# Kernel tuning notes

Hardware: AMD Instinct MI355X
Metric: run time of the kernel (lower is better)

Reference implementation:

```python
import jax, jax.numpy as jnp
import numpy as np

N = 128            # grid points per dim (periodic)
BS = 32            # batch size
MAX_ITERS = 8      # outer hybrid-solver iterations
HINTS_PERIOD = 4   # ML expert used every 4th iteration (HINTS schedule)
HIDDEN = 64        # CNN hidden channels
H = 1.0 / N        # grid spacing


def _laplacian(u):
    # periodic 5-point Laplacian on [..., N, N]
    return (
        jnp.roll(u, 1, axis=-1) + jnp.roll(u, -1, axis=-1)
        + jnp.roll(u, 1, axis=-2) + jnp.roll(u, -1, axis=-2)
        - 4.0 * u
    ) / (H * H)


def _pconv(x, w, b):
    # periodic-padded 3x3 conv, NCHW / OIHW
    xp = jnp.pad(x, ((0, 0), (0, 0), (1, 1), (1, 1)), mode='wrap')
    y = jax.lax.conv_general_dilated(xp, w, (1, 1), 'VALID',
                                     dimension_numbers=('NCHW', 'OIHW', 'NCHW'))
    return y + b[None, :, None, None]


def _cnn(x, w1, b1, w2, b2, w3, b3):
    # ML expert: residual [bs,1,N,N] -> correction [bs,1,N,N]
    h = jax.nn.relu(_pconv(x, w1, b1))
    h = jax.nn.relu(_pconv(h, w2, b2))
    return _pconv(h, w3, b3)


def setup_inputs() -> dict:
    key = jax.random.key(0)
    ks = jax.random.split(key, 7)
    f = jax.random.normal(ks[0], (BS, N, N), dtype=jnp.float32)
    u0 = jnp.zeros((BS, N, N), dtype=jnp.float32)
    s1 = 1.0 / np.sqrt(1 * 9)
    s2 = 1.0 / np.sqrt(HIDDEN * 9)
    w1 = jax.random.normal(ks[1], (HIDDEN, 1, 3, 3), jnp.float32) * s1
    b1 = jnp.zeros((HIDDEN,), jnp.float32)
    w2 = jax.random.normal(ks[2], (HIDDEN, HIDDEN, 3, 3), jnp.float32) * s2
    b2 = jnp.zeros((HIDDEN,), jnp.float32)
    w3 = jax.random.normal(ks[3], (1, HIDDEN, 3, 3), jnp.float32) * s2
    b3 = jnp.zeros((1,), jnp.float32)
    return {'f': f, 'u0': u0, 'w1': w1, 'b1': b1, 'w2': w2, 'b2': b2,
            'w3': w3, 'b3': b3}


def reference(f, u0, w1, b1, w2, b2, w3, b3):
    one_hot_ml = jnp.array([0.0, 1.0], dtype=jnp.float32)
    one_hot_num = jnp.array([1.0, 0.0], dtype=jnp.float32)

    def step(u, it):
        # residual of -lap(u) = f  ->  r = f + lap(u)
        res = f + _laplacian(u)
        # expert 0: one Jacobi sweep (diag of -lap is 4/h^2)
        u_num = u + (H * H / 4.0) * res
        # expert 1: ML correction on residual
        u_ml = u + _cnn(res[:, None], w1, b1, w2, b2, w3, b3)[:, 0]
        # HINTS router: ML every HINTS_PERIOD-th iteration, same for all samples
        use_ml = (it % HINTS_PERIOD) == (HINTS_PERIOD - 1)
        u_new = jnp.where(use_ml, u_ml, u_num)
        scores = jnp.broadcast_to(
            jnp.where(use_ml, one_hot_ml, one_hot_num)[None, :], (BS, 2))
        return u_new, (u_new, scores)

    _, (predictions, routing_scores) = jax.lax.scan(
        step, u0, jnp.arange(MAX_ITERS))
    # predictions: [max_iters, bs, N, N]; routing_scores: [max_iters, bs, 2]
    return predictions, routing_scores
```

## Files before the change

### kernel.cpp

```cpp
#include <hip/hip_runtime.h>
#include <hip/hip_bf16.h>

#define BS 32
#define SPAT 16384
#define NMASK 127

using short8  = __attribute__((ext_vector_type(8))) short;
using short4v = __attribute__((ext_vector_type(4))) short;
using f32x16  = __attribute__((ext_vector_type(16))) float;
using f32x4   = __attribute__((ext_vector_type(4))) float;

__device__ inline short f2bf(float f) {
  __hip_bfloat16 h = __float2bfloat16(f);
  return *reinterpret_cast<short*>(&h);
}

__global__ __launch_bounds__(256) void prep_kernel(
    const float* __restrict__ w2, const float* __restrict__ w1,
    const float* __restrict__ w3, short* __restrict__ w2b,
    short* __restrict__ w1a, short* __restrict__ w3b) {
  int idx = blockIdx.x * 256 + threadIdx.x;
  if (idx < 36864) {
    int cob = idx / 18432, r = idx % 18432;
    int t = r / 2048, r2 = r & 2047;
    int c = r2 >> 9, lh = (r2 >> 8) & 1, l31 = (r2 >> 3) & 31, j = r2 & 7;
    int co = cob * 32 + l31, ci = c * 16 + 8 * lh + j;
    w2b[idx] = f2bf(w2[(co * 64 + ci) * 9 + t]);
  } else if (idx < 37888) {
    int j = idx - 36864;
    int ch = j >> 4, t = j & 15;
    w1a[j] = (t < 9) ? f2bf(w1[ch * 9 + t]) : (short)0;
  } else if (idx < 39936) {
    int q = idx - 37888;
    int c = q >> 9, lh = (q >> 8) & 1, l31 = (q >> 3) & 31, j = q & 7;
    int t = l31, ci = c * 16 + 8 * lh + j;
    w3b[q] = (t < 9) ? f2bf(w3[ci * 9 + t]) : (short)0;
  }
}

__global__ __launch_bounds__(256) void jac3_kernel(
    const float* __restrict__ uin, const float* __restrict__ f,
    float* __restrict__ u1o, float* __restrict__ u2o,
    float* __restrict__ u3o, float* __restrict__ res_ws) {
  __shared__ float As[576];
  __shared__ float Bs[484];
  __shared__ float Fs[484];
  int tid = threadIdx.x;
  int bl = blockIdx.x >> 6, tile = blockIdx.x & 63;
  int y0 = (tile >> 3) << 4, x0 = (tile & 7) << 4;
  const float* ub = uin + ((size_t)bl << 14);
  const float* fb = f + ((size_t)bl << 14);
  for (int i = tid; i < 576; i += 256) {
    int uy = i / 24, ux = i % 24;
    As[i] = ub[(((y0 + uy - 4) & NMASK) << 7) + ((x0 + ux - 4) & NMASK)];
  }
  for (int i = tid; i < 484; i += 256) {
    int uy = i / 22, ux = i % 22;
    Fs[i] = fb[(((y0 + uy - 3) & NMASK) << 7) + ((x0 + ux - 3) & NMASK)];
  }
  __syncthreads();
  for (int i = tid; i < 484; i += 256) {
    int yy = i / 22, xx = i % 22;
    float uc = As[(yy + 1) * 24 + xx + 1];
    float ns = As[yy * 24 + xx + 1] + As[(yy + 2) * 24 + xx + 1]
             + As[(yy + 1) * 24 + xx] + As[(yy + 1) * 24 + xx + 2];
    Bs[i] = uc + Fs[i] * (1.f / 65536.f) + (ns - 4.f * uc) * 0.25f;
  }
  __syncthreads();
  {
    int y = tid >> 4, x = tid & 15;
    u1o[((size_t)bl << 14) + ((y0 + y) << 7) + x0 + x] = Bs[(y + 3) * 22 + x + 3];
  }
  for (int i = tid; i < 400; i += 256) {
    int yy = i / 20, xx = i % 20;
    float uc = Bs[(yy + 1) * 22 + xx + 1];
    float ns = Bs[yy * 22 + xx + 1] + Bs[(yy + 2) * 22 + xx + 1]
             + Bs[(yy + 1) * 22 + xx] + Bs[(yy + 1) * 22 + xx + 2];
    As[i] = uc + Fs[(yy + 1) * 22 + xx + 1] * (1.f / 65536.f)
          + (ns - 4.f * uc) * 0.25f;
  }
  __syncthreads();
  {
    int y = tid >> 4, x = tid & 15;
    u2o[((size_t)bl << 14) + ((y0 + y) << 7) + x0 + x] = As[(y + 2) * 20 + x + 2];
  }
  for (int i = tid; i < 324; i += 256) {
    int yy = i / 18, xx = i % 18;
    float uc = As[(yy + 1) * 20 + xx + 1];
    float ns = As[yy * 20 + xx + 1] + As[(yy + 2) * 20 + xx + 1]
             + As[(yy + 1) * 20 + xx] + As[(yy + 1) * 20 + xx + 2];
    Bs[i] = uc + Fs[(yy + 2) * 22 + xx + 2] * (1.f / 65536.f)
          + (ns - 4.f * uc) * 0.25f;
  }
  __syncthreads();
  {
    int y = tid >> 4, x = tid & 15;
    size_t gi = ((size_t)bl << 14) + ((y0 + y) << 7) + x0 + x;
    float uc = Bs[(y + 1) * 18 + x + 1];
    u3o[gi] = uc;
    float ns = Bs[y * 18 + x + 1] + Bs[(y + 2) * 18 + x + 1]
             + Bs[(y + 1) * 18 + x] + Bs[(y + 1) * 18 + x + 2];
    res_ws[gi] = Fs[(y + 3) * 22 + x + 3] + (ns - 4.f * uc) * 16384.f;
  }
}

__global__ __launch_bounds__(512, 6) void mlstep_a(
    const float* __restrict__ res_ws,
    const short* __restrict__ w1a, const float* __restrict__ b1v,
    const short* __restrict__ w2b, const float* __restrict__ b2v,
    const short* __restrict__ w3b, float* __restrict__ D_ws,
    int b0, int BC) {
  __shared__ __align__(16) short h1g[8 * 324 * 8];
  __shared__ float res_s[400];
  int tid = threadIdx.x;
  int bl = blockIdx.x >> 6;
  int tile = blockIdx.x & 63;
  int y0 = (tile >> 3) << 4, x0 = (tile & 7) << 4;
  const float* rb = res_ws + ((size_t)(b0 + bl) << 14);

  if (tid < 400) {
    int ry = tid / 20, rx = tid % 20;
    res_s[tid] = rb[(((y0 + ry - 2) & NMASK) << 7) + ((x0 + rx - 2) & NMASK)];
  }
  __syncthreads();

  int lane = tid & 63, wv = tid >> 6;
  int l31 = lane & 31, lh = lane >> 5;

  {
    short8 a1lo = *reinterpret_cast<const short8*>(&w1a[l31 * 16 + 8 * lh]);
    short8 a1hi = *reinterpret_cast<const short8*>(&w1a[(32 + l31) * 16 + 8 * lh]);
    for (int g = wv; g < 11; g += 8) {
      int pos = g * 32 + l31;
      short8 bf = {};
      if (pos < 324) {
        int yy = pos / 18, xx = pos % 18;
        if (lh == 0) {
#pragma unroll
          for (int t = 0; t < 8; ++t)
            bf[t] = f2bf(res_s[(yy + t / 3) * 20 + xx + t % 3]);
        } else {
          bf[0] = f2bf(res_s[(yy + 2) * 20 + xx + 2]);
        }
      }
      f32x16 acc0, acc1;
#pragma unroll
      for (int r = 0; r < 16; ++r) { acc0[r] = 0.f; acc1[r] = 0.f; }
      acc0 = __builtin_amdgcn_mfma_f32_32x32x16_bf16(a1lo, bf, acc0, 0, 0, 0);
      acc1 = __builtin_amdgcn_mfma_f32_32x32x16_bf16(a1hi, bf, acc1, 0, 0, 0);
      if (pos < 324) {
#pragma unroll
        for (int q = 0; q < 4; ++q) {
          f32x4 bv0 = *reinterpret_cast<const f32x4*>(&b1v[8 * q + 4 * lh]);
          f32x4 bv1 = *reinterpret_cast<const f32x4*>(&b1v[32 + 8 * q + 4 * lh]);
          short4v o0, o1;
#pragma unroll
          for (int j = 0; j < 4; ++j) {
            float v0 = acc0[4 * q + j] + bv0[j];
            float v1 = acc1[4 * q + j] + bv1[j];
            o0[j] = f2bf(v0 > 0.f ? v0 : 0.f);
            o1[j] = f2bf(v1 > 0.f ? v1 : 0.f);
          }
          *reinterpret_cast<short4v*>(
              (char*)h1g + (q * 324 + pos) * 16 + 8 * lh) = o0;
          *reinterpret_cast<short4v*>(
              (char*)h1g + ((4 + q) * 324 + pos) * 16 + 8 * lh) = o1;
        }
      }
    }
  }
  __syncthreads();

  int px = (wv << 5) + l31;
  {
    int pos0 = (px >> 4) * 18 + (px & 15);
    const char* hb = (const char*)h1g + lh * 5184 + pos0 * 16;
    const char* wb = (const char*)w2b + lane * 16;
    f32x16 acc0, acc1;
#pragma unroll
    for (int r = 0; r < 16; ++r) { acc0[r] = 0.f; acc1[r] = 0.f; }
#pragma unroll
    for (int t = 0; t < 9; ++t) {
#pragma unroll
      for (int c = 0; c < 4; ++c) {
        short8 af0 = *reinterpret_cast<const short8*>(wb + (t * 4 + c) * 1024);
        short8 af1 = *reinterpret_cast<const short8*>(
            wb + ((9 + t) * 4 + c) * 1024);
        short8 bf = *reinterpret_cast<const short8*>(
            hb + c * 10368 + ((t / 3) * 18 + (t % 3)) * 16);
        acc0 = __builtin_amdgcn_mfma_f32_32x32x16_bf16(af0, bf, acc0, 0, 0, 0);
        acc1 = __builtin_amdgcn_mfma_f32_32x32x16_bf16(af1, bf, acc1, 0, 0, 0);
      }
    }
    __syncthreads();

    short* h2t = h1g;
#pragma unroll
    for (int cb = 0; cb < 2; ++cb) {
      const f32x16& a = cb ? acc1 : acc0;
#pragma unroll
      for (int q = 0; q < 4; ++q) {
        int ch0 = cb * 32 + 8 * q + 4 * lh;
        f32x4 bv = *reinterpret_cast<const f32x4*>(&b2v[ch0]);
        short4v o;
#pragma unroll
        for (int j = 0; j < 4; ++j) {
          float v = a[4 * q + j] + bv[j];
          o[j] = f2bf(v > 0.f ? v : 0.f);
        }
        int cg = cb * 4 + q;
        *reinterpret_cast<short4v*>(&h2t[(cg * 256 + px) * 8 + 4 * lh]) = o;
      }
    }
    f32x16 d;
#pragma unroll
    for (int r = 0; r < 16; ++r) d[r] = 0.f;
#pragma unroll
    for (int c = 0; c < 4; ++c) {
      short8 af3 = *reinterpret_cast<const short8*>(
          (const char*)w3b + c * 1024 + lane * 16);
      short8 bf = *reinterpret_cast<const short8*>(
          (const char*)h2t + ((2 * c + lh) * 256 + px) * 16);
      d = __builtin_amdgcn_mfma_f32_32x32x16_bf16(af3, bf, d, 0, 0, 0);
    }
    int gpx = ((y0 + (px >> 4)) << 7) + x0 + (px & 15);
    if (lh == 0) {
#pragma unroll
      for (int r = 0; r < 4; ++r)
        D_ws[((size_t)(r * BC + bl) << 14) + gpx] = d[r];
      D_ws[((size_t)(8 * BC + bl) << 14) + gpx] = d[4];
    } else {
#pragma unroll
      for (int r = 0; r < 4; ++r)
        D_ws[((size_t)((4 + r) * BC + bl) << 14) + gpx] = d[r];
    }
  }
}

__global__ __launch_bounds__(256) void mlstep_b(
    const float* __restrict__ D_ws, const float* __restrict__ b3,
    const float* __restrict__ uprev, float* __restrict__ uout,
    int b0, int BC) {
  int idx = blockIdx.x * 256 + threadIdx.x;
  int bl = idx >> 14;
  int rem = idx & (SPAT - 1);
  int y = rem >> 7, x = rem & NMASK;
  float acc = b3[0];
#pragma unroll
  for (int t = 0; t < 9; ++t) {
    int yy = (y + t / 3 - 1) & NMASK;
    int xx = (x + t % 3 - 1) & NMASK;
    acc += D_ws[((size_t)(t * BC + bl) << 14) + (yy << 7) + xx];
  }
  size_t g = ((size_t)(b0 + bl) << 14) + rem;
  uout[g] = uprev[g] + acc;
}

__global__ void scores_kernel(float* __restrict__ s) {
  int i = blockIdx.x * 256 + threadIdx.x;
  if (i < 8 * BS * 2) {
    int it = i >> 6;
    int k = i & 1;
    bool ml = (it & 3) == 3;
    s[i] = ml ? (float)k : (float)(1 - k);
  }
}

extern "C" void kernel_launch(void* const* d_in, const int* in_sizes, int n_in,
                              void* d_out, int out_size, void* d_ws,
                              size_t ws_size, hipStream_t stream) {
  (void)in_sizes; (void)n_in; (void)out_size;
  const float* f  = (const float*)d_in[0];
  const float* u0 = (const float*)d_in[1];
  const float* w1 = (const float*)d_in[2];
  const float* b1 = (const float*)d_in[3];
  const float* w2 = (const float*)d_in[4];
  const float* b2 = (const float*)d_in[5];
  const float* w3 = (const float*)d_in[6];
  const float* b3 = (const float*)d_in[7];

  float* preds  = (float*)d_out;
  float* scores = preds + (size_t)8 * BS * SPAT;

  short* w2b = (short*)d_ws;
  short* w1a = w2b + 36864;
  short* w3b = w1a + 1024;
  float* res_ws = (float*)(w3b + 2048);
  float* D_ws = res_ws + (size_t)BS * SPAT;
  size_t fixed = (size_t)(36864 + 1024 + 2048) * 2 + (size_t)BS * SPAT * 4;
  size_t avail = ws_size > fixed ? ws_size - fixed : 0;
  int BC = 32;
  while (BC > 1 && (size_t)BC * ((size_t)9 * SPAT * 4) > avail) BC >>= 1;

  prep_kernel<<<156, 256, 0, stream>>>(w2, w1, w3, w2b, w1a, w3b);

  for (int p = 0; p < 2; ++p) {
    int it = 4 * p;
    const float* up = (p == 0) ? u0 : preds + (size_t)3 * BS * SPAT;
    float* u1o = preds + (size_t)(it + 0) * BS * SPAT;
    float* u2o = preds + (size_t)(it + 1) * BS * SPAT;
    float* u3o = preds + (size_t)(it + 2) * BS * SPAT;
    float* umo = preds + (size_t)(it + 3) * BS * SPAT;
    jac3_kernel<<<BS * 64, 256, 0, stream>>>(up, f, u1o, u2o, u3o, res_ws);
    for (int b0 = 0; b0 < BS; b0 += BC) {
      mlstep_a<<<BC * 64, 512, 0, stream>>>(res_ws, w1a, b1, w2b, b2, w3b,
                                            D_ws, b0, BC);
      mlstep_b<<<BC * SPAT / 256, 256, 0, stream>>>(D_ws, b3, u3o, umo, b0, BC);
    }
  }
  scores_kernel<<<2, 256, 0, stream>>>(scores);
}
```

Before: 142.6 us.

## Halve mlstep_a block size, give each wave two pixel tiles to reuse weight fragments

mlstep_a now runs with 256 threads (4 waves) instead of 512. Each wave computes two 32-pixel N-tiles, so every weight A-fragment loaded from global memory feeds four MFMAs instead of two. The w3 fragments are hoisted and reused across both tiles. This halves the weight-load traffic per output but doubles accumulator registers (four f32x16 per thread) and reduces wave-level parallelism per block, which may lower occupancy.

```diff
diff --git a/kernel.cpp b/kernel.cpp
--- a/kernel.cpp
+++ b/kernel.cpp
@@ -104,7 +104,7 @@
   }
 }
 
-__global__ __launch_bounds__(512, 6) void mlstep_a(
+__global__ __launch_bounds__(256, 3) void mlstep_a(
     const float* __restrict__ res_ws,
     const short* __restrict__ w1a, const float* __restrict__ b1v,
     const short* __restrict__ w2b, const float* __restrict__ b2v,
@@ -118,9 +118,9 @@
   int y0 = (tile >> 3) << 4, x0 = (tile & 7) << 4;
   const float* rb = res_ws + ((size_t)(b0 + bl) << 14);
 
-  if (tid < 400) {
-    int ry = tid / 20, rx = tid % 20;
-    res_s[tid] = rb[(((y0 + ry - 2) & NMASK) << 7) + ((x0 + rx - 2) & NMASK)];
+  for (int i = tid; i < 400; i += 256) {
+    int ry = i / 20, rx = i % 20;
+    res_s[i] = rb[(((y0 + ry - 2) & NMASK) << 7) + ((x0 + rx - 2) & NMASK)];
   }
   __syncthreads();
 
@@ -130,7 +130,7 @@
   {
     short8 a1lo = *reinterpret_cast<const short8*>(&w1a[l31 * 16 + 8 * lh]);
     short8 a1hi = *reinterpret_cast<const short8*>(&w1a[(32 + l31) * 16 + 8 * lh]);
-    for (int g = wv; g < 11; g += 8) {
+    for (int g = wv; g < 11; g += 4) {
       int pos = g * 32 + l31;
       short8 bf = {};
       if (pos < 324) {
@@ -171,14 +171,22 @@
   }
   __syncthreads();
 
-  int px = (wv << 5) + l31;
-  {
-    int pos0 = (px >> 4) * 18 + (px & 15);
-    const char* hb = (const char*)h1g + lh * 5184 + pos0 * 16;
+  {
+    const char* hb[2];
+#pragma unroll
+    for (int nt = 0; nt < 2; ++nt) {
+      int px = (wv << 6) + (nt << 5) + l31;
+      int pos0 = (px >> 4) * 18 + (px & 15);
+      hb[nt] = (const char*)h1g + lh * 5184 + pos0 * 16;
+    }
     const char* wb = (const char*)w2b + lane * 16;
-    f32x16 acc0, acc1;
-#pragma unroll
-    for (int r = 0; r < 16; ++r) { acc0[r] = 0.f; acc1[r] = 0.f; }
+    f32x16 acc[2][2];
+#pragma unroll
+    for (int cb = 0; cb < 2; ++cb)
+#pragma unroll
+      for (int nt = 0; nt < 2; ++nt)
+#pragma unroll
+        for (int r = 0; r < 16; ++r) acc[cb][nt][r] = 0.f;
 #pragma unroll
     for (int t = 0; t < 9; ++t) {
 #pragma unroll
@@ -186,53 +194,70 @@
         short8 af0 = *reinterpret_cast<const short8*>(wb + (t * 4 + c) * 1024);
         short8 af1 = *reinterpret_cast<const short8*>(
             wb + ((9 + t) * 4 + c) * 1024);
+        int toff = ((t / 3) * 18 + (t % 3)) * 16;
+#pragma unroll
+        for (int nt = 0; nt < 2; ++nt) {
+          short8 bf = *reinterpret_cast<const short8*>(
+              hb[nt] + c * 10368 + toff);
+          acc[0][nt] = __builtin_amdgcn_mfma_f32_32x32x16_bf16(af0, bf,
+                                                               acc[0][nt], 0, 0, 0);
+          acc[1][nt] = __builtin_amdgcn_mfma_f32_32x32x16_bf16(af1, bf,
+                                                               acc[1][nt], 0, 0, 0);
+        }
+      }
+    }
+    __syncthreads();
+
+    short* h2t = h1g;
+#pragma unroll
+    for (int nt = 0; nt < 2; ++nt) {
+      int px = (wv << 6) + (nt << 5) + l31;
+#pragma unroll
+      for (int cb = 0; cb < 2; ++cb) {
+#pragma unroll
+        for (int q = 0; q < 4; ++q) {
+          int ch0 = cb * 32 + 8 * q + 4 * lh;
+          f32x4 bv = *reinterpret_cast<const f32x4*>(&b2v[ch0]);
+          short4v o;
+#pragma unroll
+          for (int j = 0; j < 4; ++j) {
+            float v = acc[cb][nt][4 * q + j] + bv[j];
+            o[j] = f2bf(v > 0.f ? v : 0.f);
+          }
+          int cg = cb * 4 + q;
+          *reinterpret_cast<short4v*>(&h2t[(cg * 256 + px) * 8 + 4 * lh]) = o;
+        }
+      }
+    }
+    short8 af3[4];
+#pragma unroll
+    for (int c = 0; c < 4; ++c)
+      af3[c] = *reinterpret_cast<const short8*>(
+          (const char*)w3b + c * 1024 + lane * 16);
+#pragma unroll
+    for (int nt = 0; nt < 2; ++nt) {
+      int pxb = (wv << 6) + (nt << 5);
+      f32x16 d;
+#pragma unroll
+      for (int r = 0; r < 16; ++r) d[r] = 0.f;
+#pragma unroll
+      for (int c = 0; c < 4; ++c) {
         short8 bf = *reinterpret_cast<const short8*>(
-            hb + c * 10368 + ((t / 3) * 18 + (t % 3)) * 16);
-        acc0 = __builtin_amdgcn_mfma_f32_32x32x16_bf16(af0, bf, acc0, 0, 0, 0);
-        acc1 = __builtin_amdgcn_mfma_f32_32x32x16_bf16(af1, bf, acc1, 0, 0, 0);
-      }
-    }
-    __syncthreads();
-
-    short* h2t = h1g;
-#pragma unroll
-    for (int cb = 0; cb < 2; ++cb) {
-      const f32x16& a = cb ? acc1 : acc0;
-#pragma unroll
-      for (int q = 0; q < 4; ++q) {
-        int ch0 = cb * 32 + 8 * q + 4 * lh;
-        f32x4 bv = *reinterpret_cast<const f32x4*>(&b2v[ch0]);
-        short4v o;
-#pragma unroll
-        for (int j = 0; j < 4; ++j) {
-          float v = a[4 * q + j] + bv[j];
-          o[j] = f2bf(v > 0.f ? v : 0.f);
-        }
-        int cg = cb * 4 + q;
-        *reinterpret_cast<short4v*>(&h2t[(cg * 256 + px) * 8 + 4 * lh]) = o;
-      }
-    }
-    f32x16 d;
-#pragma unroll
-    for (int r = 0; r < 16; ++r) d[r] = 0.f;
-#pragma unroll
-    for (int c = 0; c < 4; ++c) {
-      short8 af3 = *reinterpret_cast<const short8*>(
-          (const char*)w3b + c * 1024 + lane * 16);
-      short8 bf = *reinterpret_cast<const short8*>(
-          (const char*)h2t + ((2 * c + lh) * 256 + px) * 16);
-      d = __builtin_amdgcn_mfma_f32_32x32x16_bf16(af3, bf, d, 0, 0, 0);
-    }
-    int gpx = ((y0 + (px >> 4)) << 7) + x0 + (px & 15);
-    if (lh == 0) {
-#pragma unroll
-      for (int r = 0; r < 4; ++r)
-        D_ws[((size_t)(r * BC + bl) << 14) + gpx] = d[r];
-      D_ws[((size_t)(8 * BC + bl) << 14) + gpx] = d[4];
-    } else {
-#pragma unroll
-      for (int r = 0; r < 4; ++r)
-        D_ws[((size_t)((4 + r) * BC + bl) << 14) + gpx] = d[r];
+            (const char*)h2t + ((2 * c + lh) * 256 + pxb + l31) * 16);
+        d = __builtin_amdgcn_mfma_f32_32x32x16_bf16(af3[c], bf, d, 0, 0, 0);
+      }
+      int px = pxb + l31;
+      int gpx = ((y0 + (px >> 4)) << 7) + x0 + (px & 15);
+      if (lh == 0) {
+#pragma unroll
+        for (int r = 0; r < 4; ++r)
+          D_ws[((size_t)(r * BC + bl) << 14) + gpx] = d[r];
+        D_ws[((size_t)(8 * BC + bl) << 14) + gpx] = d[4];
+      } else {
+#pragma unroll
+        for (int r = 0; r < 4; ++r)
+          D_ws[((size_t)((4 + r) * BC + bl) << 14) + gpx] = d[r];
+      }
     }
   }
 }
@@ -303,7 +328,7 @@
     float* umo = preds + (size_t)(it + 3) * BS * SPAT;
     jac3_kernel<<<BS * 64, 256, 0, stream>>>(up, f, u1o, u2o, u3o, res_ws);
     for (int b0 = 0; b0 < BS; b0 += BC) {
-      mlstep_a<<<BC * 64, 512, 0, stream>>>(res_ws, w1a, b1, w2b, b2, w3b,
+      mlstep_a<<<BC * 64, 256, 0, stream>>>(res_ws, w1a, b1, w2b, b2, w3b,
                                             D_ws, b0, BC);
       mlstep_b<<<BC * SPAT / 256, 256, 0, stream>>>(D_ws, b3, u3o, umo, b0, BC);
     }
```

Measured after the change: 137.1 us. 3.9% less time.

## Halve mlstep_a waves, double per-wave pixel tile with prefetched weight registers

Applied to the files above, without the earlier changes.

The conv2 stage in mlstep_a now runs 4 waves per block instead of 8, and each wave computes two 32-pixel N-tiles, so every weight fragment loaded from global memory is reused across two MFMAs. Weight fragments are triple-buffered in registers, and the loads for later taps are issued before the MFMAs of the current tap; the first two taps are prefetched before the first barrier. s_setprio is raised around the MFMA bursts. The cost is much higher register pressure, which cuts occupancy (launch bounds 256,3), plus fewer waves available to hide LDS latency.

```diff
diff --git a/kernel.cpp b/kernel.cpp
--- a/kernel.cpp
+++ b/kernel.cpp
@@ -104,7 +104,34 @@
   }
 }
 
-__global__ __launch_bounds__(512, 6) void mlstep_a(
+#define WDECL(S) short8 S##0, S##1, S##2, S##3, S##4, S##5, S##6, S##7
+#define WLOAD(S, T) do {                                                   \
+  S##0 = *reinterpret_cast<const short8*>(wb + ((T) * 4 + 0) * 1024);      \
+  S##1 = *reinterpret_cast<const short8*>(wb + ((T) * 4 + 1) * 1024);      \
+  S##2 = *reinterpret_cast<const short8*>(wb + ((T) * 4 + 2) * 1024);      \
+  S##3 = *reinterpret_cast<const short8*>(wb + ((T) * 4 + 3) * 1024);      \
+  S##4 = *reinterpret_cast<const short8*>(wb + ((9 + (T)) * 4 + 0) * 1024);\
+  S##5 = *reinterpret_cast<const short8*>(wb + ((9 + (T)) * 4 + 1) * 1024);\
+  S##6 = *reinterpret_cast<const short8*>(wb + ((9 + (T)) * 4 + 2) * 1024);\
+  S##7 = *reinterpret_cast<const short8*>(wb + ((9 + (T)) * 4 + 3) * 1024);\
+} while (0)
+#define WMFMA_C(S, A, B, C) do {                                           \
+  short8 bf0 = *reinterpret_cast<const short8*>(hb0 + (C) * 10368 + toff); \
+  short8 bf1 = *reinterpret_cast<const short8*>(hb1 + (C) * 10368 + toff); \
+  acc00 = __builtin_amdgcn_mfma_f32_32x32x16_bf16(S##A, bf0, acc00, 0,0,0);\
+  acc01 = __builtin_amdgcn_mfma_f32_32x32x16_bf16(S##A, bf1, acc01, 0,0,0);\
+  acc10 = __builtin_amdgcn_mfma_f32_32x32x16_bf16(S##B, bf0, acc10, 0,0,0);\
+  acc11 = __builtin_amdgcn_mfma_f32_32x32x16_bf16(S##B, bf1, acc11, 0,0,0);\
+} while (0)
+#define WMFMA(S, T) do {                                                   \
+  int toff = (((T) / 3) * 18 + ((T) % 3)) * 16;                            \
+  __builtin_amdgcn_s_setprio(1);                                           \
+  WMFMA_C(S, 0, 4, 0); WMFMA_C(S, 1, 5, 1);                                \
+  WMFMA_C(S, 2, 6, 2); WMFMA_C(S, 3, 7, 3);                                \
+  __builtin_amdgcn_s_setprio(0);                                           \
+} while (0)
+
+__global__ __launch_bounds__(256, 3) void mlstep_a(
     const float* __restrict__ res_ws,
     const short* __restrict__ w1a, const float* __restrict__ b1v,
     const short* __restrict__ w2b, const float* __restrict__ b2v,
@@ -118,19 +145,24 @@
   int y0 = (tile >> 3) << 4, x0 = (tile & 7) << 4;
   const float* rb = res_ws + ((size_t)(b0 + bl) << 14);
 
-  if (tid < 400) {
-    int ry = tid / 20, rx = tid % 20;
-    res_s[tid] = rb[(((y0 + ry - 2) & NMASK) << 7) + ((x0 + rx - 2) & NMASK)];
-  }
-  __syncthreads();
+  for (int i = tid; i < 400; i += 256) {
+    int ry = i / 20, rx = i % 20;
+    res_s[i] = rb[(((y0 + ry - 2) & NMASK) << 7) + ((x0 + rx - 2) & NMASK)];
+  }
 
   int lane = tid & 63, wv = tid >> 6;
   int l31 = lane & 31, lh = lane >> 5;
 
+  const char* wb = (const char*)w2b + lane * 16;
+  WDECL(wA); WDECL(wB); WDECL(wC);
+  WLOAD(wA, 0);
+  WLOAD(wB, 1);
+  __syncthreads();
+
   {
     short8 a1lo = *reinterpret_cast<const short8*>(&w1a[l31 * 16 + 8 * lh]);
     short8 a1hi = *reinterpret_cast<const short8*>(&w1a[(32 + l31) * 16 + 8 * lh]);
-    for (int g = wv; g < 11; g += 8) {
+    for (int g = wv; g < 11; g += 4) {
       int pos = g * 32 + l31;
       short8 bf = {};
       if (pos < 324) {
@@ -171,68 +203,92 @@
   }
   __syncthreads();
 
-  int px = (wv << 5) + l31;
-  {
-    int pos0 = (px >> 4) * 18 + (px & 15);
-    const char* hb = (const char*)h1g + lh * 5184 + pos0 * 16;
-    const char* wb = (const char*)w2b + lane * 16;
-    f32x16 acc0, acc1;
-#pragma unroll
-    for (int r = 0; r < 16; ++r) { acc0[r] = 0.f; acc1[r] = 0.f; }
-#pragma unroll
-    for (int t = 0; t < 9; ++t) {
-#pragma unroll
-      for (int c = 0; c < 4; ++c) {
-        short8 af0 = *reinterpret_cast<const short8*>(wb + (t * 4 + c) * 1024);
-        short8 af1 = *reinterpret_cast<const short8*>(
-            wb + ((9 + t) * 4 + c) * 1024);
-        short8 bf = *reinterpret_cast<const short8*>(
-            hb + c * 10368 + ((t / 3) * 18 + (t % 3)) * 16);
-        acc0 = __builtin_amdgcn_mfma_f32_32x32x16_bf16(af0, bf, acc0, 0, 0, 0);
-        acc1 = __builtin_amdgcn_mfma_f32_32x32x16_bf16(af1, bf, acc1, 0, 0, 0);
-      }
-    }
+  {
+    const char* hb0;
+    const char* hb1;
+    {
+      int px0 = (wv << 6) + l31;
+      int px1 = (wv << 6) + 32 + l31;
+      hb0 = (const char*)h1g + lh * 5184 + ((px0 >> 4) * 18 + (px0 & 15)) * 16;
+      hb1 = (const char*)h1g + lh * 5184 + ((px1 >> 4) * 18 + (px1 & 15)) * 16;
+    }
+    f32x16 acc00, acc01, acc10, acc11;
+#pragma unroll
+    for (int r = 0; r < 16; ++r) {
+      acc00[r] = 0.f; acc01[r] = 0.f; acc10[r] = 0.f; acc11[r] = 0.f;
+    }
+    WLOAD(wC, 2); WMFMA(wA, 0);
+    WLOAD(wA, 3); WMFMA(wB, 1);
+    WLOAD(wB, 4); WMFMA(wC, 2);
+    WLOAD(wC, 5); WMFMA(wA, 3);
+    WLOAD(wA, 6); WMFMA(wB, 4);
+    WLOAD(wB, 7); WMFMA(wC, 5);
+    WLOAD(wC, 8); WMFMA(wA, 6);
+    WMFMA(wB, 7);
+    WMFMA(wC, 8);
     __syncthreads();
 
     short* h2t = h1g;
 #pragma unroll
-    for (int cb = 0; cb < 2; ++cb) {
-      const f32x16& a = cb ? acc1 : acc0;
-#pragma unroll
-      for (int q = 0; q < 4; ++q) {
-        int ch0 = cb * 32 + 8 * q + 4 * lh;
-        f32x4 bv = *reinterpret_cast<const f32x4*>(&b2v[ch0]);
-        short4v o;
-#pragma unroll
-        for (int j = 0; j < 4; ++j) {
-          float v = a[4 * q + j] + bv[j];
-          o[j] = f2bf(v > 0.f ? v : 0.f);
+    for (int nt = 0; nt < 2; ++nt) {
+      int px = (wv << 6) + (nt << 5) + l31;
+#pragma unroll
+      for (int cb = 0; cb < 2; ++cb) {
+        const f32x16& a = cb ? (nt ? acc11 : acc10) : (nt ? acc01 : acc00);
+#pragma unroll
+        for (int q = 0; q < 4; ++q) {
+          int ch0 = cb * 32 + 8 * q + 4 * lh;
+          f32x4 bv = *reinterpret_cast<const f32x4*>(&b2v[ch0]);
+          short4v o;
+#pragma unroll
+          for (int j = 0; j < 4; ++j) {
+            float v = a[4 * q + j] + bv[j];
+            o[j] = f2bf(v > 0.f ? v : 0.f);
+          }
+          int cg = cb * 4 + q;
+          *reinterpret_cast<short4v*>(&h2t[(cg * 256 + px) * 8 + 4 * lh]) = o;
         }
-        int cg = cb * 4 + q;
-        *reinterpret_cast<short4v*>(&h2t[(cg * 256 + px) * 8 + 4 * lh]) = o;
-      }
-    }
-    f32x16 d;
-#pragma unroll
-    for (int r = 0; r < 16; ++r) d[r] = 0.f;
-#pragma unroll
-    for (int c = 0; c < 4; ++c) {
-      short8 af3 = *reinterpret_cast<const short8*>(
-          (const char*)w3b + c * 1024 + lane * 16);
-      short8 bf = *reinterpret_cast<const short8*>(
-          (const char*)h2t + ((2 * c + lh) * 256 + px) * 16);
-      d = __builtin_amdgcn_mfma_f32_32x32x16_bf16(af3, bf, d, 0, 0, 0);
-    }
-    int gpx = ((y0 + (px >> 4)) << 7) + x0 + (px & 15);
-    if (lh == 0) {
-#pragma unroll
-      for (int r = 0; r < 4; ++r)
-        D_ws[((size_t)(r * BC + bl) << 14) + gpx] = d[r];
-      D_ws[((size_t)(8 * BC + bl) << 14) + gpx] = d[4];
-    } else {
-#pragma unroll
-      for (int r = 0; r < 4; ++r)
-        D_ws[((size_t)((4 + r) * BC + bl) << 14) + gpx] = d[r];
+      }
+    }
+    short8 af30 = *reinterpret_cast<const short8*>((const char*)w3b + lane * 16);
+    short8 af31 = *reinterpret_cast<const short8*>((const char*)w3b + 1024 + lane * 16);
+    short8 af32 = *reinterpret_cast<const short8*>((const char*)w3b + 2048 + lane * 16);
+    short8 af33 = *reinterpret_cast<const short8*>((const char*)w3b + 3072 + lane * 16);
+#pragma unroll
+    for (int nt = 0; nt < 2; ++nt) {
+      int pxb = (wv << 6) + (nt << 5);
+      f32x16 d;
+#pragma unroll
+      for (int r = 0; r < 16; ++r) d[r] = 0.f;
+      __builtin_amdgcn_s_setprio(1);
+      {
+        short8 bf;
+        bf = *reinterpret_cast<const short8*>(
+            (const char*)h2t + ((0 + lh) * 256 + pxb + l31) * 16);
+        d = __builtin_amdgcn_mfma_f32_32x32x16_bf16(af30, bf, d, 0, 0, 0);
+        bf = *reinterpret_cast<const short8*>(
+            (const char*)h2t + ((2 + lh) * 256 + pxb + l31) * 16);
+        d = __builtin_amdgcn_mfma_f32_32x32x16_bf16(af31, bf, d, 0, 0, 0);
+        bf = *reinterpret_cast<const short8*>(
+            (const char*)h2t + ((4 + lh) * 256 + pxb + l31) * 16);
+        d = __builtin_amdgcn_mfma_f32_32x32x16_bf16(af32, bf, d, 0, 0, 0);
+        bf = *reinterpret_cast<const short8*>(
+            (const char*)h2t + ((6 + lh) * 256 + pxb + l31) * 16);
+        d = __builtin_amdgcn_mfma_f32_32x32x16_bf16(af33, bf, d, 0, 0, 0);
+      }
+      __builtin_amdgcn_s_setprio(0);
+      int px = pxb + l31;
+      int gpx = ((y0 + (px >> 4)) << 7) + x0 + (px & 15);
+      if (lh == 0) {
+#pragma unroll
+        for (int r = 0; r < 4; ++r)
+          D_ws[((size_t)(r * BC + bl) << 14) + gpx] = d[r];
+        D_ws[((size_t)(8 * BC + bl) << 14) + gpx] = d[4];
+      } else {
+#pragma unroll
+        for (int r = 0; r < 4; ++r)
+          D_ws[((size_t)((4 + r) * BC + bl) << 14) + gpx] = d[r];
+      }
     }
   }
 }
@@ -303,7 +359,7 @@
     float* umo = preds + (size_t)(it + 3) * BS * SPAT;
     jac3_kernel<<<BS * 64, 256, 0, stream>>>(up, f, u1o, u2o, u3o, res_ws);
     for (int b0 = 0; b0 < BS; b0 += BC) {
-      mlstep_a<<<BC * 64, 512, 0, stream>>>(res_ws, w1a, b1, w2b, b2, w3b,
+      mlstep_a<<<BC * 64, 256, 0, stream>>>(res_ws, w1a, b1, w2b, b2, w3b,
                                             D_ws, b0, BC);
       mlstep_b<<<BC * SPAT / 256, 256, 0, stream>>>(D_ws, b3, u3o, umo, b0, BC);
     }
```

Result: slower. 162.5 us (+13.9%).
